# Optimization experiments

Measured on AMD Instinct MI355X. Metric: run time of the kernel, lower is better.

The kernel has to match this reference:

```python
import jax, jax.numpy as jnp
import numpy as np
from jax import lax

N, D, H, E = 8192, 1024, 4096, 8


def setup_inputs() -> dict:
    key = jax.random.key(0)
    ks = jax.random.split(key, 7)
    s = 0.02
    return {
        "x": jax.random.normal(ks[0], (N, D), dtype=jnp.float32),
        "Wr": jax.random.normal(ks[1], (E, D), dtype=jnp.float32) * s,
        "br": jnp.zeros((E,), dtype=jnp.float32),
        "Wup": jax.random.normal(ks[2], (E, H, D), dtype=jnp.float32) * s,
        "bup": jnp.zeros((E, H), dtype=jnp.float32),
        "Wdown": jax.random.normal(ks[3], (E, D, H), dtype=jnp.float32) * s,
        "bdown": jnp.zeros((E, D), dtype=jnp.float32),
    }


def reference(x, Wr, br, Wup, bup, Wdown, bdown):
    # Router: softmax over logits; only argmax is used (softmax is monotone,
    # argmax of softmax == argmax of logits).
    logits = x @ Wr.T + br            # [N, E]
    scores = jax.nn.softmax(logits, axis=-1)
    top1 = jnp.argmax(scores, axis=-1)  # [N] int

    out0 = jnp.zeros_like(x)

    def body(out, ew):
        i, Wu, bu, Wd, bd = ew
        h = jax.nn.silu(x @ Wu.T + bu)   # [N, H]
        y = h @ Wd.T + bd                # [N, D]
        out = jnp.where((top1 == i)[:, None], y, out)
        return out, None

    idx = jnp.arange(Wup.shape[0])
    out, _ = lax.scan(body, out0, (idx, Wup, bup, Wdown, bdown))
    return out
```

## Files before the change

### kernel.cpp

```cpp
#include <hip/hip_runtime.h>

#define NT 8192
#define DD 1024
#define HH 4096
#define EE 8

typedef __attribute__((ext_vector_type(8))) short short8;
typedef __attribute__((ext_vector_type(4))) float f32x4;

__device__ __forceinline__ unsigned short f2bf(float f) {
    unsigned int u = __float_as_uint(f);
    u += 0x7FFFu + ((u >> 16) & 1u);
    return (unsigned short)(u >> 16);
}

__device__ __forceinline__ void gload_lds16(const void* g, void* l) {
    __builtin_amdgcn_global_load_lds(
        (const __attribute__((address_space(1))) unsigned int*)g,
        (__attribute__((address_space(3))) unsigned int*)l, 16, 0, 0);
}

__global__ __launch_bounds__(256) void cvtw_kernel(const float* __restrict__ a,
                                                   const float* __restrict__ b,
                                                   unsigned short* __restrict__ da,
                                                   unsigned short* __restrict__ db) {
    const size_t half = (size_t)EE * HH * DD;
    size_t i = ((size_t)blockIdx.x * 256 + threadIdx.x) * 4;
    const float* s; unsigned short* d;
    if (i < half) { s = a + i; d = da + i; }
    else          { s = b + (i - half); d = db + (i - half); }
    float4 v = *(const float4*)s;
    ushort4 o;
    o.x = f2bf(v.x); o.y = f2bf(v.y); o.z = f2bf(v.z); o.w = f2bf(v.w);
    *(ushort4*)d = o;
}

__global__ __launch_bounds__(256) void router_kernel(const float* __restrict__ x,
                                                     const float* __restrict__ Wr,
                                                     const float* __restrict__ br,
                                                     int* __restrict__ counts,
                                                     int* __restrict__ tlist) {
    __shared__ float sW[EE * DD];
    const int t = threadIdx.x;
    for (int i = t; i < EE * DD / 4; i += 256)
        ((float4*)sW)[i] = ((const float4*)Wr)[i];
    __syncthreads();
    const int lane = t & 63;
    const int wv = t >> 6;
    const int token = blockIdx.x * 4 + wv;
    const float* xr = x + (size_t)token * DD;
    float acc[EE];
#pragma unroll
    for (int e = 0; e < EE; e++) acc[e] = 0.f;
    for (int k = lane; k < DD; k += 64) {
        float xv = xr[k];
#pragma unroll
        for (int e = 0; e < EE; e++) acc[e] += xv * sW[e * DD + k];
    }
#pragma unroll
    for (int off = 32; off > 0; off >>= 1) {
#pragma unroll
        for (int e = 0; e < EE; e++) acc[e] += __shfl_xor(acc[e], off);
    }
    if (lane == 0) {
        int best = 0;
        float bv = acc[0] + br[0];
#pragma unroll
        for (int e = 1; e < EE; e++) {
            float v = acc[e] + br[e];
            if (v > bv) { bv = v; best = e; }
        }
        int pos = atomicAdd(&counts[best], 1);
        tlist[best * NT + pos] = token;
    }
}

__global__ void offsets_kernel(const int* __restrict__ counts, int* __restrict__ offsets) {
    if (threadIdx.x == 0) {
        int s = 0;
        for (int e = 0; e < EE; e++) { offsets[e] = s; s += counts[e]; }
    }
}

__global__ __launch_bounds__(256) void gather_kernel(const float* __restrict__ x,
                                                     const int* __restrict__ tlist,
                                                     const int* __restrict__ offsets,
                                                     unsigned short* __restrict__ xg) {
    const int row = blockIdx.x * 4 + (threadIdx.x >> 6);
    const int lane = threadIdx.x & 63;
    int e = 0;
#pragma unroll
    for (int k = 1; k < EE; k++)
        if (row >= offsets[k]) e = k;
    const int token = tlist[e * NT + row - offsets[e]];
    const float4* src = (const float4*)(x + (size_t)token * DD);
    ushort4* dst = (ushort4*)(xg + (size_t)row * DD);
#pragma unroll
    for (int it = 0; it < 4; it++) {
        float4 v = src[it * 64 + lane];
        ushort4 o;
        o.x = f2bf(v.x); o.y = f2bf(v.y); o.z = f2bf(v.z); o.w = f2bf(v.w);
        dst[it * 64 + lane] = o;
    }
}

__global__ __launch_bounds__(256) void up_gemm(const unsigned short* __restrict__ xg,
                                               const unsigned short* __restrict__ Wub,
                                               const float* __restrict__ bup,
                                               const int* __restrict__ counts,
                                               const int* __restrict__ offsets,
                                               unsigned short* __restrict__ hbuf) {
    const int e = blockIdx.z;
    const int cnt = counts[e];
    const int m0 = blockIdx.y * 128;
    if (m0 >= cnt) return;
    const int n0 = blockIdx.x * 128;
    const int t = threadIdx.x;
    const int off_e = offsets[e];

    __shared__ unsigned short sA[128 * 32];
    __shared__ unsigned short sB[128 * 32];

    const int r0 = t >> 2;
    const int kc = t & 3;
    const int c1 = cnt - 1;
    int ra = m0 + r0;      if (ra > c1) ra = c1;
    int rb = m0 + 64 + r0; if (rb > c1) rb = c1;
    const unsigned short* gA0 = xg + (size_t)(off_e + ra) * DD + kc * 8;
    const unsigned short* gA1 = xg + (size_t)(off_e + rb) * DD + kc * 8;
    const unsigned short* gB0 = Wub + ((size_t)e * HH + n0 + r0) * DD + kc * 8;
    const unsigned short* gB1 = Wub + ((size_t)e * HH + n0 + 64 + r0) * DD + kc * 8;
    unsigned short* lA0 = sA + t * 8;
    unsigned short* lA1 = sA + (t + 256) * 8;
    unsigned short* lB0 = sB + t * 8;
    unsigned short* lB1 = sB + (t + 256) * 8;

    const int lane = t & 63;
    const int wm = ((t >> 6) & 1) * 64;
    const int wn = (t >> 7) * 64;
    const int mrow = lane & 15;
    const int kq = lane >> 4;

    f32x4 acc[4][4];
#pragma unroll
    for (int i = 0; i < 4; i++)
#pragma unroll
        for (int j = 0; j < 4; j++)
            acc[i][j] = (f32x4){0.f, 0.f, 0.f, 0.f};

    for (int kt = 0; kt < DD; kt += 32) {
        __syncthreads();
        gload_lds16(gA0 + kt, lA0);
        gload_lds16(gA1 + kt, lA1);
        gload_lds16(gB0 + kt, lB0);
        gload_lds16(gB1 + kt, lB1);
        __syncthreads();
        short8 a[4], b[4];
#pragma unroll
        for (int i = 0; i < 4; i++) {
            a[i] = *(const short8*)(sA + (wm + i * 16 + mrow) * 32 + kq * 8);
            b[i] = *(const short8*)(sB + (wn + i * 16 + mrow) * 32 + kq * 8);
        }
#pragma unroll
        for (int i = 0; i < 4; i++)
#pragma unroll
            for (int j = 0; j < 4; j++)
                acc[i][j] = __builtin_amdgcn_mfma_f32_16x16x32_bf16(a[i], b[j], acc[i][j], 0, 0, 0);
    }

    float bias[4];
#pragma unroll
    for (int j = 0; j < 4; j++) bias[j] = bup[e * HH + n0 + wn + j * 16 + mrow];
#pragma unroll
    for (int i = 0; i < 4; i++) {
#pragma unroll
        for (int r = 0; r < 4; r++) {
            int m = m0 + wm + i * 16 + kq * 4 + r;
            if (m < cnt) {
                unsigned short* hrow = hbuf + (size_t)(off_e + m) * HH + n0 + wn + mrow;
#pragma unroll
                for (int j = 0; j < 4; j++) {
                    float v = acc[i][j][r] + bias[j];
                    v = v / (1.f + __expf(-v));
                    hrow[j * 16] = f2bf(v);
                }
            }
        }
    }
}

__global__ __launch_bounds__(256) void down_gemm(const unsigned short* __restrict__ hbuf,
                                                 const unsigned short* __restrict__ Wdb,
                                                 const float* __restrict__ bdown,
                                                 const int* __restrict__ counts,
                                                 const int* __restrict__ tlist,
                                                 const int* __restrict__ offsets,
                                                 float* __restrict__ out) {
    const int e = blockIdx.z >> 1;
    const int s = blockIdx.z & 1;
    const int cnt = counts[e];
    const int m0 = blockIdx.y * 128;
    if (m0 >= cnt) return;
    const int n0 = blockIdx.x * 128;
    const int t = threadIdx.x;

    __shared__ unsigned short sA[128 * 32];
    __shared__ unsigned short sB[128 * 32];

    const int r0 = t >> 2;
    const int kc = t & 3;
    const int off_e = offsets[e];
    const int c1 = cnt - 1;
    int ra = m0 + r0;      if (ra > c1) ra = c1;
    int rb = m0 + 64 + r0; if (rb > c1) rb = c1;
    const unsigned short* gA0 = hbuf + (size_t)(off_e + ra) * HH + kc * 8;
    const unsigned short* gA1 = hbuf + (size_t)(off_e + rb) * HH + kc * 8;
    const unsigned short* gB0 = Wdb + ((size_t)e * DD + n0 + r0) * HH + kc * 8;
    const unsigned short* gB1 = Wdb + ((size_t)e * DD + n0 + 64 + r0) * HH + kc * 8;
    unsigned short* lA0 = sA + t * 8;
    unsigned short* lA1 = sA + (t + 256) * 8;
    unsigned short* lB0 = sB + t * 8;
    unsigned short* lB1 = sB + (t + 256) * 8;

    const int lane = t & 63;
    const int wm = ((t >> 6) & 1) * 64;
    const int wn = (t >> 7) * 64;
    const int mrow = lane & 15;
    const int kq = lane >> 4;

    f32x4 acc[4][4];
#pragma unroll
    for (int i = 0; i < 4; i++)
#pragma unroll
        for (int j = 0; j < 4; j++)
            acc[i][j] = (f32x4){0.f, 0.f, 0.f, 0.f};

    const int kbeg = s * (HH / 2);
    const int kend = kbeg + (HH / 2);
    for (int kt = kbeg; kt < kend; kt += 32) {
        __syncthreads();
        gload_lds16(gA0 + kt, lA0);
        gload_lds16(gA1 + kt, lA1);
        gload_lds16(gB0 + kt, lB0);
        gload_lds16(gB1 + kt, lB1);
        __syncthreads();
        short8 a[4], b[4];
#pragma unroll
        for (int i = 0; i < 4; i++) {
            a[i] = *(const short8*)(sA + (wm + i * 16 + mrow) * 32 + kq * 8);
            b[i] = *(const short8*)(sB + (wn + i * 16 + mrow) * 32 + kq * 8);
        }
#pragma unroll
        for (int i = 0; i < 4; i++)
#pragma unroll
            for (int j = 0; j < 4; j++)
                acc[i][j] = __builtin_amdgcn_mfma_f32_16x16x32_bf16(a[i], b[j], acc[i][j], 0, 0, 0);
    }

    const int* tl = tlist + e * NT;
    float bias[4];
#pragma unroll
    for (int j = 0; j < 4; j++)
        bias[j] = (s == 0) ? bdown[e * DD + n0 + wn + j * 16 + mrow] : 0.f;
#pragma unroll
    for (int i = 0; i < 4; i++) {
#pragma unroll
        for (int r = 0; r < 4; r++) {
            int m = m0 + wm + i * 16 + kq * 4 + r;
            if (m < cnt) {
                int token = tl[m];
                float* orow = out + (size_t)token * DD + n0 + wn + mrow;
#pragma unroll
                for (int j = 0; j < 4; j++)
                    atomicAdd(&orow[j * 16], acc[i][j][r] + bias[j]);
            }
        }
    }
}

extern "C" void kernel_launch(void* const* d_in, const int* in_sizes, int n_in,
                              void* d_out, int out_size, void* d_ws, size_t ws_size,
                              hipStream_t stream) {
    const float* x     = (const float*)d_in[0];
    const float* Wr    = (const float*)d_in[1];
    const float* br    = (const float*)d_in[2];
    const float* Wup   = (const float*)d_in[3];
    const float* bup   = (const float*)d_in[4];
    const float* Wdown = (const float*)d_in[5];
    const float* bdown = (const float*)d_in[6];
    float* out = (float*)d_out;

    char* w = (char*)d_ws;
    int* counts  = (int*)w;               w += 256;
    int* offsets = (int*)w;               w += 256;
    int* tlist   = (int*)w;               w += (size_t)EE * NT * 4;
    unsigned short* xg   = (unsigned short*)w;  w += (size_t)NT * DD * 2;
    unsigned short* hbuf = (unsigned short*)w;  w += (size_t)NT * HH * 2;
    unsigned short* Wub  = (unsigned short*)w;  w += (size_t)EE * HH * DD * 2;
    unsigned short* Wdb  = (unsigned short*)w;

    hipMemsetAsync(counts, 0, EE * sizeof(int), stream);
    hipMemsetAsync(out, 0, (size_t)NT * DD * sizeof(float), stream);

    cvtw_kernel<<<(2 * (size_t)EE * HH * DD) / 1024, 256, 0, stream>>>(Wup, Wdown, Wub, Wdb);
    router_kernel<<<NT / 4, 256, 0, stream>>>(x, Wr, br, counts, tlist);
    offsets_kernel<<<1, 64, 0, stream>>>(counts, offsets);
    gather_kernel<<<NT / 4, 256, 0, stream>>>(x, tlist, offsets, xg);

    dim3 gu(HH / 128, NT / 128, EE);
    up_gemm<<<gu, 256, 0, stream>>>(xg, Wub, bup, counts, offsets, hbuf);
    dim3 gd(DD / 128, NT / 128, EE * 2);
    down_gemm<<<gd, 256, 0, stream>>>(hbuf, Wdb, bdown, counts, tlist, offsets, out);
}
```

Measured before the change: 699.8 us.

## Swizzle LDS tiles, drop split-K atomics, and fold offsets kernel into consumers

Applies an XOR swizzle to the LDS tile column chunks in both GEMMs so that fragment reads spread across banks. Removes the 2-way split-K in the down GEMM, which lets it store results directly instead of using float atomics and removes the output memset. Each consumer now computes the expert offsets inline from counts, so the single-thread offsets kernel is gone. The trade-off is half as many down-GEMM blocks, giving less parallelism, plus some redundant prefix sums per block.

```diff
diff --git a/kernel.cpp b/kernel.cpp
--- a/kernel.cpp
+++ b/kernel.cpp
@@ -75,24 +75,21 @@
     }
 }
 
-__global__ void offsets_kernel(const int* __restrict__ counts, int* __restrict__ offsets) {
-    if (threadIdx.x == 0) {
-        int s = 0;
-        for (int e = 0; e < EE; e++) { offsets[e] = s; s += counts[e]; }
-    }
-}
-
 __global__ __launch_bounds__(256) void gather_kernel(const float* __restrict__ x,
                                                      const int* __restrict__ tlist,
-                                                     const int* __restrict__ offsets,
+                                                     const int* __restrict__ counts,
                                                      unsigned short* __restrict__ xg) {
     const int row = blockIdx.x * 4 + (threadIdx.x >> 6);
     const int lane = threadIdx.x & 63;
+    int off[EE];
+    int s = 0;
+#pragma unroll
+    for (int k = 0; k < EE; k++) { off[k] = s; s += counts[k]; }
     int e = 0;
 #pragma unroll
     for (int k = 1; k < EE; k++)
-        if (row >= offsets[k]) e = k;
-    const int token = tlist[e * NT + row - offsets[e]];
+        if (row >= off[k]) e = k;
+    const int token = tlist[e * NT + row - off[e]];
     const float4* src = (const float4*)(x + (size_t)token * DD);
     ushort4* dst = (ushort4*)(xg + (size_t)row * DD);
 #pragma unroll
@@ -104,25 +101,30 @@
     }
 }
 
+
 __global__ __launch_bounds__(256) void up_gemm(const unsigned short* __restrict__ xg,
                                                const unsigned short* __restrict__ Wub,
                                                const float* __restrict__ bup,
                                                const int* __restrict__ counts,
-                                               const int* __restrict__ offsets,
                                                unsigned short* __restrict__ hbuf) {
     const int e = blockIdx.z;
-    const int cnt = counts[e];
+    int off_e = 0, cnt;
+    {
+        int s = 0;
+#pragma unroll
+        for (int k = 0; k < EE; k++) { if (k == e) off_e = s; s += counts[k]; }
+        cnt = counts[e];
+    }
     const int m0 = blockIdx.y * 128;
     if (m0 >= cnt) return;
     const int n0 = blockIdx.x * 128;
     const int t = threadIdx.x;
-    const int off_e = offsets[e];
 
     __shared__ unsigned short sA[128 * 32];
     __shared__ unsigned short sB[128 * 32];
 
     const int r0 = t >> 2;
-    const int kc = t & 3;
+    const int kc = (t & 3) ^ ((r0 >> 1) & 3);
     const int c1 = cnt - 1;
     int ra = m0 + r0;      if (ra > c1) ra = c1;
     int rb = m0 + 64 + r0; if (rb > c1) rb = c1;
@@ -140,6 +142,7 @@
     const int wn = (t >> 7) * 64;
     const int mrow = lane & 15;
     const int kq = lane >> 4;
+    const int slot = (kq ^ ((mrow >> 1) & 3)) * 8;
 
     f32x4 acc[4][4];
 #pragma unroll
@@ -158,8 +161,8 @@
         short8 a[4], b[4];
 #pragma unroll
         for (int i = 0; i < 4; i++) {
-            a[i] = *(const short8*)(sA + (wm + i * 16 + mrow) * 32 + kq * 8);
-            b[i] = *(const short8*)(sB + (wn + i * 16 + mrow) * 32 + kq * 8);
+            a[i] = *(const short8*)(sA + (wm + i * 16 + mrow) * 32 + slot);
+            b[i] = *(const short8*)(sB + (wn + i * 16 + mrow) * 32 + slot);
         }
 #pragma unroll
         for (int i = 0; i < 4; i++)
@@ -194,11 +197,15 @@
                                                  const float* __restrict__ bdown,
                                                  const int* __restrict__ counts,
                                                  const int* __restrict__ tlist,
-                                                 const int* __restrict__ offsets,
                                                  float* __restrict__ out) {
-    const int e = blockIdx.z >> 1;
-    const int s = blockIdx.z & 1;
-    const int cnt = counts[e];
+    const int e = blockIdx.z;
+    int off_e = 0, cnt;
+    {
+        int s = 0;
+#pragma unroll
+        for (int k = 0; k < EE; k++) { if (k == e) off_e = s; s += counts[k]; }
+        cnt = counts[e];
+    }
     const int m0 = blockIdx.y * 128;
     if (m0 >= cnt) return;
     const int n0 = blockIdx.x * 128;
@@ -208,8 +215,7 @@
     __shared__ unsigned short sB[128 * 32];
 
     const int r0 = t >> 2;
-    const int kc = t & 3;
-    const int off_e = offsets[e];
+    const int kc = (t & 3) ^ ((r0 >> 1) & 3);
     const int c1 = cnt - 1;
     int ra = m0 + r0;      if (ra > c1) ra = c1;
     int rb = m0 + 64 + r0; if (rb > c1) rb = c1;
@@ -227,6 +233,7 @@
     const int wn = (t >> 7) * 64;
     const int mrow = lane & 15;
     const int kq = lane >> 4;
+    const int slot = (kq ^ ((mrow >> 1) & 3)) * 8;
 
     f32x4 acc[4][4];
 #pragma unroll
@@ -235,9 +242,7 @@
         for (int j = 0; j < 4; j++)
             acc[i][j] = (f32x4){0.f, 0.f, 0.f, 0.f};
 
-    const int kbeg = s * (HH / 2);
-    const int kend = kbeg + (HH / 2);
-    for (int kt = kbeg; kt < kend; kt += 32) {
+    for (int kt = 0; kt < HH; kt += 32) {
         __syncthreads();
         gload_lds16(gA0 + kt, lA0);
         gload_lds16(gA1 + kt, lA1);
@@ -247,8 +252,8 @@
         short8 a[4], b[4];
 #pragma unroll
         for (int i = 0; i < 4; i++) {
-            a[i] = *(const short8*)(sA + (wm + i * 16 + mrow) * 32 + kq * 8);
-            b[i] = *(const short8*)(sB + (wn + i * 16 + mrow) * 32 + kq * 8);
+            a[i] = *(const short8*)(sA + (wm + i * 16 + mrow) * 32 + slot);
+            b[i] = *(const short8*)(sB + (wn + i * 16 + mrow) * 32 + slot);
         }
 #pragma unroll
         for (int i = 0; i < 4; i++)
@@ -260,8 +265,7 @@
     const int* tl = tlist + e * NT;
     float bias[4];
 #pragma unroll
-    for (int j = 0; j < 4; j++)
-        bias[j] = (s == 0) ? bdown[e * DD + n0 + wn + j * 16 + mrow] : 0.f;
+    for (int j = 0; j < 4; j++) bias[j] = bdown[e * DD + n0 + wn + j * 16 + mrow];
 #pragma unroll
     for (int i = 0; i < 4; i++) {
 #pragma unroll
@@ -272,7 +276,7 @@
                 float* orow = out + (size_t)token * DD + n0 + wn + mrow;
 #pragma unroll
                 for (int j = 0; j < 4; j++)
-                    atomicAdd(&orow[j * 16], acc[i][j][r] + bias[j]);
+                    orow[j * 16] = acc[i][j][r] + bias[j];
             }
         }
     }
@@ -292,7 +296,6 @@
 
     char* w = (char*)d_ws;
     int* counts  = (int*)w;               w += 256;
-    int* offsets = (int*)w;               w += 256;
     int* tlist   = (int*)w;               w += (size_t)EE * NT * 4;
     unsigned short* xg   = (unsigned short*)w;  w += (size_t)NT * DD * 2;
     unsigned short* hbuf = (unsigned short*)w;  w += (size_t)NT * HH * 2;
@@ -300,15 +303,13 @@
     unsigned short* Wdb  = (unsigned short*)w;
 
     hipMemsetAsync(counts, 0, EE * sizeof(int), stream);
-    hipMemsetAsync(out, 0, (size_t)NT * DD * sizeof(float), stream);
 
     cvtw_kernel<<<(2 * (size_t)EE * HH * DD) / 1024, 256, 0, stream>>>(Wup, Wdown, Wub, Wdb);
     router_kernel<<<NT / 4, 256, 0, stream>>>(x, Wr, br, counts, tlist);
-    offsets_kernel<<<1, 64, 0, stream>>>(counts, offsets);
-    gather_kernel<<<NT / 4, 256, 0, stream>>>(x, tlist, offsets, xg);
+    gather_kernel<<<NT / 4, 256, 0, stream>>>(x, tlist, counts, xg);
 
     dim3 gu(HH / 128, NT / 128, EE);
-    up_gemm<<<gu, 256, 0, stream>>>(xg, Wub, bup, counts, offsets, hbuf);
-    dim3 gd(DD / 128, NT / 128, EE * 2);
-    down_gemm<<<gd, 256, 0, stream>>>(hbuf, Wdb, bdown, counts, tlist, offsets, out);
-}
+    up_gemm<<<gu, 256, 0, stream>>>(xg, Wub, bup, counts, hbuf);
+    dim3 gd(DD / 128, NT / 128, EE);
+    down_gemm<<<gd, 256, 0, stream>>>(hbuf, Wdb, bdown, counts, tlist, out);
+}
```

After: 659.0 us. 1.06x faster.
